# Performance work log

Hardware: AMD Instinct MI355X
Metric: run time of the kernel (lower is better)

The kernel has to match this reference:

```python
import jax, jax.numpy as jnp
import numpy as np

E = 1024
B, QL, KVL = 8, 2048, 2048


def setup_inputs() -> dict:
    key = jax.random.key(0)
    ks = jax.random.split(key, 12)
    s = 1.0 / np.sqrt(E)
    return {
        "query": jax.random.normal(ks[0], (B, QL, E), jnp.float32),
        "key_value": jax.random.normal(ks[1], (B, KVL, E), jnp.float32),
        "attention_mask": jax.random.randint(ks[2], (B, QL, KVL), 0, 2, jnp.int32),
        "Wq": jax.random.uniform(ks[3], (E, E), jnp.float32, -s, s),
        "bq": jax.random.uniform(ks[4], (E,), jnp.float32, -s, s),
        "Wk": jax.random.uniform(ks[5], (E, E), jnp.float32, -s, s),
        "bk": jax.random.uniform(ks[6], (E,), jnp.float32, -s, s),
        "Wv": jax.random.uniform(ks[7], (E, E), jnp.float32, -s, s),
        "bv": jax.random.uniform(ks[8], (E,), jnp.float32, -s, s),
        "Wo": jax.random.uniform(ks[9], (E, E), jnp.float32, -s, s),
        "bo": jax.random.uniform(ks[10], (E,), jnp.float32, -s, s),
    }


def reference(query, key_value, attention_mask, Wq, bq, Wk, bk, Wv, bv, Wo, bo):
    # torch Linear: x @ W.T + b
    q = jnp.einsum('bqe,fe->bqf', query, Wq) + bq          # [B, QL, E]
    k = jnp.einsum('bke,fe->bkf', key_value, Wk) + bk      # [B, KVL, E]
    v = jnp.einsum('bke,fe->bkf', key_value, Wv) + bv      # [B, KVL, E]
    scale = 1.0 / jnp.sqrt(jnp.asarray(q.shape[-1], q.dtype))
    attn = jnp.einsum('bqe,bke->bqk', q, k) * scale        # [B, QL, KVL]
    attn = jnp.where(attention_mask == 0, -jnp.inf, attn)
    attn = jax.nn.softmax(attn, axis=-1)
    out = jnp.einsum('bqk,bke->bqe', attn, v)              # [B, QL, E]
    out = jnp.einsum('bqe,fe->bqf', out, Wo) + bo
    return out
```

## Files before the change

kernel.cpp:

```cpp
#include <hip/hip_runtime.h>
#include <hip/hip_bf16.h>
#include <stdint.h>

typedef unsigned short u16;
typedef short s16x8 __attribute__((ext_vector_type(8)));
typedef u16 u16x8 __attribute__((ext_vector_type(8)));
typedef u16 u16x4 __attribute__((ext_vector_type(4)));
typedef float f32x4 __attribute__((ext_vector_type(4)));

__device__ __forceinline__ u16 f2bf(float f) {
  union { float f; uint32_t u; } c; c.f = f;
  uint32_t u = c.u;
  u = u + 0x7fffu + ((u >> 16) & 1u);
  return (u16)(u >> 16);
}
__device__ __forceinline__ float bf2f(u16 b) {
  union { uint32_t u; float f; } c; c.u = ((uint32_t)b) << 16;
  return c.f;
}

__device__ __forceinline__ void gld_lds16(const u16* g, u16* l) {
  __builtin_amdgcn_global_load_lds(
      (const __attribute__((address_space(1))) uint32_t*)g,
      (__attribute__((address_space(3))) uint32_t*)l,
      16, 0, 0);
}

__global__ __launch_bounds__(256) void cvt_wt(
    const float* __restrict__ Wq, const float* __restrict__ Wk,
    const float* __restrict__ Wv, const float* __restrict__ Wo,
    u16* __restrict__ WqT, u16* __restrict__ WkT, u16* __restrict__ WvT,
    u16* __restrict__ wo) {
  const int z = blockIdx.z;
  const int tid = threadIdx.x;
  if (z == 3) {
    const long base = ((long)(blockIdx.y * 16 + blockIdx.x)) * 4096 + tid * 16;
#pragma unroll
    for (int h = 0; h < 2; ++h) {
      const float4 a = *(const float4*)&Wo[base + h * 8];
      const float4 b = *(const float4*)&Wo[base + h * 8 + 4];
      u16x8 r;
      r[0] = f2bf(a.x); r[1] = f2bf(a.y); r[2] = f2bf(a.z); r[3] = f2bf(a.w);
      r[4] = f2bf(b.x); r[5] = f2bf(b.y); r[6] = f2bf(b.z); r[7] = f2bf(b.w);
      *(u16x8*)&wo[base + h * 8] = r;
    }
    return;
  }
  const float* src = (z == 0) ? Wq : (z == 1) ? Wk : Wv;
  u16* dst = (z == 0) ? WqT : (z == 1) ? WkT : WvT;
  __shared__ u16 t[64][66];
  const int r0 = blockIdx.x * 64, c0 = blockIdx.y * 64;
#pragma unroll
  for (int i = 0; i < 2; ++i) {
    const int ch = i * 256 + tid;
    const int r = ch >> 3, cc = ch & 7;
    const float4 a = *(const float4*)&src[(long)(r0 + r) * 1024 + c0 + cc * 8];
    const float4 b = *(const float4*)&src[(long)(r0 + r) * 1024 + c0 + cc * 8 + 4];
    t[r][cc * 8 + 0] = f2bf(a.x); t[r][cc * 8 + 1] = f2bf(a.y);
    t[r][cc * 8 + 2] = f2bf(a.z); t[r][cc * 8 + 3] = f2bf(a.w);
    t[r][cc * 8 + 4] = f2bf(b.x); t[r][cc * 8 + 5] = f2bf(b.y);
    t[r][cc * 8 + 6] = f2bf(b.z); t[r][cc * 8 + 7] = f2bf(b.w);
  }
  __syncthreads();
#pragma unroll
  for (int i = 0; i < 2; ++i) {
    const int ch = i * 256 + tid;
    const int c = ch >> 3, rr = ch & 7;
    u16x8 r8;
#pragma unroll
    for (int j = 0; j < 8; ++j) r8[j] = t[rr * 8 + j][c];
    *(u16x8*)&dst[(long)(c0 + c) * 1024 + r0 + rr * 8] = r8;
  }
}

__global__ __launch_bounds__(256) void bgemv(
    const u16* __restrict__ matA, const float* __restrict__ vecA,
    const u16* __restrict__ matB, const float* __restrict__ vecB,
    const float* __restrict__ addB, float* __restrict__ outA,
    float* __restrict__ outB, float scaleA) {
  __shared__ float w[1024];
  const int tid = threadIdx.x;
  const bool second = blockIdx.x >= 64;
  const u16* mat = second ? matB : matA;
  const float* vec = second ? vecB : vecA;
  const int rb = (second ? (int)blockIdx.x - 64 : (int)blockIdx.x) * 16;
#pragma unroll
  for (int i = 0; i < 4; ++i) w[i * 256 + tid] = vec[i * 256 + tid];
  __syncthreads();
  const int lane = tid & 63, wv_ = tid >> 6;
#pragma unroll
  for (int r = 0; r < 4; ++r) {
    const int row = rb + wv_ * 4 + r;
    const u16* p = &mat[(long)row * 1024 + lane * 16];
    const u16x8 a = *(const u16x8*)p;
    const u16x8 b = *(const u16x8*)(p + 8);
    float s = 0.f;
#pragma unroll
    for (int j = 0; j < 8; ++j) s += bf2f(a[j]) * w[lane * 16 + j];
#pragma unroll
    for (int j = 0; j < 8; ++j) s += bf2f(b[j]) * w[lane * 16 + 8 + j];
#pragma unroll
    for (int off = 32; off >= 1; off >>= 1) s += __shfl_xor(s, off);
    if (lane == 0) {
      if (second) outB[row] = s + addB[row];
      else        outA[row] = s * scaleA;
    }
  }
}

__global__ __launch_bounds__(256) void cvt_inputs(
    const float* __restrict__ kv, const float* __restrict__ query,
    const float* __restrict__ wvec, u16* __restrict__ kvbf,
    u16* __restrict__ qbf, float* __restrict__ cvec) {
  __shared__ float w[1024];
  const int tid = threadIdx.x;
  const bool qside = blockIdx.x >= 2048;
  if (!qside) {
#pragma unroll
    for (int i = 0; i < 4; ++i) w[i * 256 + tid] = wvec[i * 256 + tid];
    __syncthreads();
  }
  const int lane = tid & 63, wv_ = tid >> 6;
  const long blk = qside ? (long)blockIdx.x - 2048 : (long)blockIdx.x;
  const float* src_base = qside ? query : kv;
  u16* dst_base = qside ? qbf : kvbf;
#pragma unroll
  for (int r = 0; r < 2; ++r) {
    const long row = blk * 8 + wv_ * 2 + r;
    const float* src = &src_base[row * 1024 + lane * 16];
    const float4 a0 = *(const float4*)src;
    const float4 a1 = *(const float4*)(src + 4);
    const float4 a2 = *(const float4*)(src + 8);
    const float4 a3 = *(const float4*)(src + 12);
    u16x8 p0, p1;
    p0[0] = f2bf(a0.x); p0[1] = f2bf(a0.y); p0[2] = f2bf(a0.z); p0[3] = f2bf(a0.w);
    p0[4] = f2bf(a1.x); p0[5] = f2bf(a1.y); p0[6] = f2bf(a1.z); p0[7] = f2bf(a1.w);
    p1[0] = f2bf(a2.x); p1[1] = f2bf(a2.y); p1[2] = f2bf(a2.z); p1[3] = f2bf(a2.w);
    p1[4] = f2bf(a3.x); p1[5] = f2bf(a3.y); p1[6] = f2bf(a3.z); p1[7] = f2bf(a3.w);
    *(u16x8*)&dst_base[row * 1024 + lane * 16] = p0;
    *(u16x8*)&dst_base[row * 1024 + lane * 16 + 8] = p1;
    if (!qside) {
      const float* wl = &w[lane * 16];
      float s = a0.x * wl[0] + a0.y * wl[1] + a0.z * wl[2] + a0.w * wl[3]
              + a1.x * wl[4] + a1.y * wl[5] + a1.z * wl[6] + a1.w * wl[7]
              + a2.x * wl[8] + a2.y * wl[9] + a2.z * wl[10] + a2.w * wl[11]
              + a3.x * wl[12] + a3.y * wl[13] + a3.z * wl[14] + a3.w * wl[15];
#pragma unroll
      for (int off = 32; off >= 1; off >>= 1) s += __shfl_xor(s, off);
      if (lane == 0) cvec[row] = s;
    }
  }
}

__global__ __launch_bounds__(256) void softmax_rows(u16* __restrict__ S) {
  const long base = (long)blockIdx.x * 2048;
  const int tid = threadIdx.x;
  const int lane = tid & 63, wave = tid >> 6;
  u16x8 raw = *(const u16x8*)&S[base + tid * 8];
  float v[8];
#pragma unroll
  for (int j = 0; j < 8; ++j) v[j] = bf2f(raw[j]);
  float m = v[0];
#pragma unroll
  for (int j = 1; j < 8; ++j) m = fmaxf(m, v[j]);
#pragma unroll
  for (int off = 32; off >= 1; off >>= 1) m = fmaxf(m, __shfl_xor(m, off));
  __shared__ float red[8];
  if (lane == 0) red[wave] = m;
  __syncthreads();
  m = fmaxf(fmaxf(red[0], red[1]), fmaxf(red[2], red[3]));
  float s = 0.f;
#pragma unroll
  for (int j = 0; j < 8; ++j) { v[j] = __expf(v[j] - m); s += v[j]; }
#pragma unroll
  for (int off = 32; off >= 1; off >>= 1) s += __shfl_xor(s, off);
  if (lane == 0) red[4 + wave] = s;
  __syncthreads();
  s = (red[4] + red[5]) + (red[6] + red[7]);
  const float inv = 1.f / s;
#pragma unroll
  for (int j = 0; j < 8; ++j) raw[j] = f2bf(v[j] * inv);
  *(u16x8*)&S[base + tid * 8] = raw;
}

union __align__(16) SmemT {
  u16 stage[2][128 * 64];
  float epi[32 * 132];
};

__device__ __forceinline__ s16x8 ldsfrag(const u16* p, int r, int c8) {
  return *(const s16x8*)&p[r * 64 + ((c8 ^ (r & 7)) << 3)];
}

__device__ __forceinline__ void stage128(const u16* __restrict__ gb, int row0,
                                         int K, int k0, u16* lbuf, int tid) {
#pragma unroll
  for (int i = 0; i < 4; ++i) {
    const int f = i * 256 + tid;
    const int rl = f >> 3, s = f & 7;
    const int gc = (s ^ (rl & 7)) << 3;
    gld_lds16(gb + (long)(row0 + rl) * K + k0 + gc, lbuf + f * 8);
  }
}

template<bool HAS_BIAS, int MODE, bool HAS_MASK>
__global__ __launch_bounds__(256, 4) void gemm128(
    const u16* __restrict__ A, const u16* __restrict__ B,
    const float* __restrict__ bias, const int* __restrict__ mask,
    void* __restrict__ Cv,
    int M, int N, int K, long sA, long sB, long sC, long sMask, long sBias,
    float scale) {
  __shared__ SmemT sm;
  const int nx = gridDim.x, ny = gridDim.y;
  const int did = blockIdx.x + nx * (blockIdx.y + ny * blockIdx.z);
  const int cpx = (nx * ny * gridDim.z) >> 3;
  const int nf = (did & 7) * cpx + (did >> 3);
  const int b = nf / (nx * ny);
  const int rr = nf % (nx * ny);
  const int bm = (rr / ny) * 128;
  const int bn = (rr % ny) * 128;

  const u16* Ab = A + (long)b * sA;
  const u16* Bb = B + (long)b * sB;
  const float* biasB = HAS_BIAS ? (bias + (long)b * sBias) : nullptr;
  const int tid = threadIdx.x;
  const int lane = tid & 63, wave = tid >> 6;
  const int wm = wave >> 1, wn = wave & 1;
  const int lr = lane & 15, lk = lane >> 4;
  const int NT = K >> 6;

  f32x4 acc[4][4] = {};

  for (int t = 0; t < NT; ++t) {
    stage128(Ab, bm, K, t << 6, sm.stage[0], tid);
    stage128(Bb, bn, K, t << 6, sm.stage[1], tid);
    asm volatile("s_waitcnt vmcnt(0)" ::: "memory");
    __syncthreads();
#pragma unroll
    for (int ks = 0; ks < 2; ++ks) {
      s16x8 af[4], bg[4];
#pragma unroll
      for (int mi = 0; mi < 4; ++mi)
        af[mi] = ldsfrag(sm.stage[0], wm * 64 + mi * 16 + lr, ks * 4 + lk);
#pragma unroll
      for (int ni = 0; ni < 4; ++ni)
        bg[ni] = ldsfrag(sm.stage[1], wn * 64 + ni * 16 + lr, ks * 4 + lk);
#pragma unroll
      for (int mi = 0; mi < 4; ++mi)
#pragma unroll
        for (int ni = 0; ni < 4; ++ni)
          acc[mi][ni] = __builtin_amdgcn_mfma_f32_16x16x32_bf16(
              af[mi], bg[ni], acc[mi][ni], 0, 0, 0);
    }
    __syncthreads();
  }

  const long cb = (long)b * sC;
  const int q = tid & 7, r = tid >> 3;
#pragma unroll
  for (int h = 0; h < 4; ++h) {
    __syncthreads();
    if (wm == (h >> 1)) {
      const int mi0 = (h & 1) * 2;
#pragma unroll
      for (int mm = 0; mm < 2; ++mm) {
        const int mi = mi0 + mm;
#pragma unroll
        for (int ni = 0; ni < 4; ++ni) {
          const int c = wn * 64 + ni * 16 + lr;
          const float bvx = HAS_BIAS ? biasB[bn + c] : 0.f;
#pragma unroll
          for (int j = 0; j < 4; ++j)
            sm.epi[(mm * 16 + (lk << 2) + j) * 132 + c] =
                acc[mi][ni][j] * scale + bvx;
        }
      }
    }
    __syncthreads();
    const int growi = bm + h * 32 + r;
    const long grow = cb + (long)growi * N + bn;
    const long mrow = HAS_MASK
        ? ((long)b * sMask + (long)growi * (long)N + bn) : 0;
#pragma unroll
    for (int ch = 0; ch < 2; ++ch) {
      const int c0 = ch * 64 + q * 8;
      const float4 x = *(const float4*)&sm.epi[r * 132 + c0];
      const float4 y = *(const float4*)&sm.epi[r * 132 + c0 + 4];
      if (MODE == 1) {
        *(float4*)&((float*)Cv)[grow + c0] = x;
        *(float4*)&((float*)Cv)[grow + c0 + 4] = y;
      } else {
        u16x8 pk;
        if (HAS_MASK) {
          const int4 ma = *(const int4*)&mask[mrow + c0];
          const int4 mb = *(const int4*)&mask[mrow + c0 + 4];
          pk[0] = f2bf(ma.x ? x.x : -1e30f);
          pk[1] = f2bf(ma.y ? x.y : -1e30f);
          pk[2] = f2bf(ma.z ? x.z : -1e30f);
          pk[3] = f2bf(ma.w ? x.w : -1e30f);
          pk[4] = f2bf(mb.x ? y.x : -1e30f);
          pk[5] = f2bf(mb.y ? y.y : -1e30f);
          pk[6] = f2bf(mb.z ? y.z : -1e30f);
          pk[7] = f2bf(mb.w ? y.w : -1e30f);
        } else {
          pk[0] = f2bf(x.x); pk[1] = f2bf(x.y);
          pk[2] = f2bf(x.z); pk[3] = f2bf(x.w);
          pk[4] = f2bf(y.x); pk[5] = f2bf(y.y);
          pk[6] = f2bf(y.z); pk[7] = f2bf(y.w);
        }
        *(u16x8*)&((u16*)Cv)[grow + c0] = pk;
      }
    }
  }
}

extern "C" void kernel_launch(void* const* d_in, const int* in_sizes, int n_in,
                              void* d_out, int out_size, void* d_ws, size_t ws_size,
                              hipStream_t stream) {
  const float* query = (const float*)d_in[0];
  const float* kv    = (const float*)d_in[1];
  const int*   mask  = (const int*)d_in[2];
  const float* Wq = (const float*)d_in[3];
  const float* bq = (const float*)d_in[4];
  const float* Wk = (const float*)d_in[5];
  const float* bk = (const float*)d_in[6];
  const float* Wv = (const float*)d_in[7];
  const float* bv = (const float*)d_in[8];
  const float* Wo = (const float*)d_in[9];
  const float* bo = (const float*)d_in[10];
  float* out = (float*)d_out;
  (void)bk;

  char* ws = (char*)d_ws;
  const size_t MB = (size_t)1 << 20;
  u16* qbf  = (u16*)(ws + 0);
  u16* kvbf = (u16*)(ws + 32 * MB);
  u16* wo   = (u16*)(ws + 70 * MB);
  u16* WqT  = (u16*)(ws + 72 * MB);
  u16* WkT  = (u16*)(ws + 74 * MB);
  u16* WvT  = (u16*)(ws + 76 * MB);
  u16* Mt   = (u16*)(ws + 78 * MB);
  u16* Wvo  = (u16*)(ws + 80 * MB);
  float* wvec = (float*)(ws + 82 * MB);
  float* bvo  = (float*)(ws + 82 * MB + 65536);
  float* cvec = (float*)(ws + 83 * MB);
  u16* qM   = (u16*)(ws + 84 * MB);
  u16* VwT  = (u16*)(ws + 116 * MB);
  u16* S    = (u16*)(ws + 148 * MB);

  const long sQK = (long)2048 * 1024;
  const long sS  = (long)2048 * 2048;

  cvt_wt<<<dim3(16, 16, 4), 256, 0, stream>>>(Wq, Wk, Wv, Wo,
                                              WqT, WkT, WvT, wo);
  bgemv<<<128, 256, 0, stream>>>(WkT, bq, wo, bv, bo, wvec, bvo, 0.03125f);

  cvt_inputs<<<4096, 256, 0, stream>>>(kv, query, wvec, kvbf, qbf, cvec);

  gemm128<false, 0, false><<<dim3(8, 8, 2), 256, 0, stream>>>(
      WkT, WqT, nullptr, nullptr, Mt, 1024, 1024, 1024,
      -2097152L, 2097152L, 1048576L, 0, 0, 1.f);

  gemm128<false, 0, false><<<dim3(128, 8, 1), 256, 0, stream>>>(
      qbf, Mt, nullptr, nullptr, qM, 16384, 1024, 1024, 0, 0, 0, 0, 0, 1.f);

  gemm128<false, 0, false><<<dim3(8, 16, 8), 256, 0, stream>>>(
      Wvo, kvbf, nullptr, nullptr, VwT, 1024, 2048, 1024,
      0, sQK, sQK, 0, 0, 1.f);

  gemm128<true, 0, true><<<dim3(16, 16, 8), 256, 0, stream>>>(
      qM, kvbf, cvec, mask, S, 2048, 2048, 1024, sQK, sQK, sS, sS, 2048,
      0.03125f);

  softmax_rows<<<16384, 256, 0, stream>>>(S);

  gemm128<true, 1, false><<<dim3(16, 8, 8), 256, 0, stream>>>(
      S, VwT, bvo, nullptr, out, 2048, 1024, 2048, sS, sQK, sQK, 0, 0, 1.f);
}
```

Baseline: 333.1 us.

## Merge independent prep kernels into two heterogeneous fused launches

Replaces five separate launches (bgemv, cvt_inputs, the Mt GEMM, the qM GEMM and the VwT GEMM) with two kernels that dispatch by block index. One handles input conversion, the Mt GEMM and the bias GEMVs; the other handles the qM and VwT GEMMs plus the cvec GEMV, now computed from bf16 kv instead of fp32. The aim is to cut launch gaps and let independent work fill the GPU together. In exchange, every block now uses GEMM-sized shared memory, which may reduce occupancy for the light conversion blocks. cvec also loses precision because it is built from bf16 inputs.

```diff
diff --git a/kernel.cpp b/kernel.cpp
--- a/kernel.cpp
+++ b/kernel.cpp
@@ -5,7 +5,6 @@
 typedef unsigned short u16;
 typedef short s16x8 __attribute__((ext_vector_type(8)));
 typedef u16 u16x8 __attribute__((ext_vector_type(8)));
-typedef u16 u16x4 __attribute__((ext_vector_type(4)));
 typedef float f32x4 __attribute__((ext_vector_type(4)));
 
 __device__ __forceinline__ u16 f2bf(float f) {
@@ -73,85 +72,6 @@
   }
 }
 
-__global__ __launch_bounds__(256) void bgemv(
-    const u16* __restrict__ matA, const float* __restrict__ vecA,
-    const u16* __restrict__ matB, const float* __restrict__ vecB,
-    const float* __restrict__ addB, float* __restrict__ outA,
-    float* __restrict__ outB, float scaleA) {
-  __shared__ float w[1024];
-  const int tid = threadIdx.x;
-  const bool second = blockIdx.x >= 64;
-  const u16* mat = second ? matB : matA;
-  const float* vec = second ? vecB : vecA;
-  const int rb = (second ? (int)blockIdx.x - 64 : (int)blockIdx.x) * 16;
-#pragma unroll
-  for (int i = 0; i < 4; ++i) w[i * 256 + tid] = vec[i * 256 + tid];
-  __syncthreads();
-  const int lane = tid & 63, wv_ = tid >> 6;
-#pragma unroll
-  for (int r = 0; r < 4; ++r) {
-    const int row = rb + wv_ * 4 + r;
-    const u16* p = &mat[(long)row * 1024 + lane * 16];
-    const u16x8 a = *(const u16x8*)p;
-    const u16x8 b = *(const u16x8*)(p + 8);
-    float s = 0.f;
-#pragma unroll
-    for (int j = 0; j < 8; ++j) s += bf2f(a[j]) * w[lane * 16 + j];
-#pragma unroll
-    for (int j = 0; j < 8; ++j) s += bf2f(b[j]) * w[lane * 16 + 8 + j];
-#pragma unroll
-    for (int off = 32; off >= 1; off >>= 1) s += __shfl_xor(s, off);
-    if (lane == 0) {
-      if (second) outB[row] = s + addB[row];
-      else        outA[row] = s * scaleA;
-    }
-  }
-}
-
-__global__ __launch_bounds__(256) void cvt_inputs(
-    const float* __restrict__ kv, const float* __restrict__ query,
-    const float* __restrict__ wvec, u16* __restrict__ kvbf,
-    u16* __restrict__ qbf, float* __restrict__ cvec) {
-  __shared__ float w[1024];
-  const int tid = threadIdx.x;
-  const bool qside = blockIdx.x >= 2048;
-  if (!qside) {
-#pragma unroll
-    for (int i = 0; i < 4; ++i) w[i * 256 + tid] = wvec[i * 256 + tid];
-    __syncthreads();
-  }
-  const int lane = tid & 63, wv_ = tid >> 6;
-  const long blk = qside ? (long)blockIdx.x - 2048 : (long)blockIdx.x;
-  const float* src_base = qside ? query : kv;
-  u16* dst_base = qside ? qbf : kvbf;
-#pragma unroll
-  for (int r = 0; r < 2; ++r) {
-    const long row = blk * 8 + wv_ * 2 + r;
-    const float* src = &src_base[row * 1024 + lane * 16];
-    const float4 a0 = *(const float4*)src;
-    const float4 a1 = *(const float4*)(src + 4);
-    const float4 a2 = *(const float4*)(src + 8);
-    const float4 a3 = *(const float4*)(src + 12);
-    u16x8 p0, p1;
-    p0[0] = f2bf(a0.x); p0[1] = f2bf(a0.y); p0[2] = f2bf(a0.z); p0[3] = f2bf(a0.w);
-    p0[4] = f2bf(a1.x); p0[5] = f2bf(a1.y); p0[6] = f2bf(a1.z); p0[7] = f2bf(a1.w);
-    p1[0] = f2bf(a2.x); p1[1] = f2bf(a2.y); p1[2] = f2bf(a2.z); p1[3] = f2bf(a2.w);
-    p1[4] = f2bf(a3.x); p1[5] = f2bf(a3.y); p1[6] = f2bf(a3.z); p1[7] = f2bf(a3.w);
-    *(u16x8*)&dst_base[row * 1024 + lane * 16] = p0;
-    *(u16x8*)&dst_base[row * 1024 + lane * 16 + 8] = p1;
-    if (!qside) {
-      const float* wl = &w[lane * 16];
-      float s = a0.x * wl[0] + a0.y * wl[1] + a0.z * wl[2] + a0.w * wl[3]
-              + a1.x * wl[4] + a1.y * wl[5] + a1.z * wl[6] + a1.w * wl[7]
-              + a2.x * wl[8] + a2.y * wl[9] + a2.z * wl[10] + a2.w * wl[11]
-              + a3.x * wl[12] + a3.y * wl[13] + a3.z * wl[14] + a3.w * wl[15];
-#pragma unroll
-      for (int off = 32; off >= 1; off >>= 1) s += __shfl_xor(s, off);
-      if (lane == 0) cvec[row] = s;
-    }
-  }
-}
-
 __global__ __launch_bounds__(256) void softmax_rows(u16* __restrict__ S) {
   const long base = (long)blockIdx.x * 2048;
   const int tid = threadIdx.x;
@@ -204,16 +124,13 @@
 }
 
 template<bool HAS_BIAS, int MODE, bool HAS_MASK>
-__global__ __launch_bounds__(256, 4) void gemm128(
-    const u16* __restrict__ A, const u16* __restrict__ B,
+__device__ __forceinline__ void gemm128_body(
+    SmemT& sm, int tid, const u16* __restrict__ A, const u16* __restrict__ B,
     const float* __restrict__ bias, const int* __restrict__ mask,
-    void* __restrict__ Cv,
-    int M, int N, int K, long sA, long sB, long sC, long sMask, long sBias,
-    float scale) {
-  __shared__ SmemT sm;
-  const int nx = gridDim.x, ny = gridDim.y;
-  const int did = blockIdx.x + nx * (blockIdx.y + ny * blockIdx.z);
-  const int cpx = (nx * ny * gridDim.z) >> 3;
+    void* __restrict__ Cv, int M, int N, int K,
+    long sA, long sB, long sC, long sMask, long sBias, float scale,
+    int did, int nx, int ny, int nz) {
+  const int cpx = (nx * ny * nz) >> 3;
   const int nf = (did & 7) * cpx + (did >> 3);
   const int b = nf / (nx * ny);
   const int rr = nf % (nx * ny);
@@ -223,7 +140,6 @@
   const u16* Ab = A + (long)b * sA;
   const u16* Bb = B + (long)b * sB;
   const float* biasB = HAS_BIAS ? (bias + (long)b * sBias) : nullptr;
-  const int tid = threadIdx.x;
   const int lane = tid & 63, wave = tid >> 6;
   const int wm = wave >> 1, wn = wave & 1;
   const int lr = lane & 15, lk = lane >> 4;
@@ -314,6 +230,131 @@
   }
 }
 
+template<bool HAS_BIAS, int MODE, bool HAS_MASK>
+__global__ __launch_bounds__(256, 4) void gemm128(
+    const u16* __restrict__ A, const u16* __restrict__ B,
+    const float* __restrict__ bias, const int* __restrict__ mask,
+    void* __restrict__ Cv,
+    int M, int N, int K, long sA, long sB, long sC, long sMask, long sBias,
+    float scale) {
+  __shared__ SmemT sm;
+  const int did = blockIdx.x + gridDim.x * (blockIdx.y + gridDim.y * blockIdx.z);
+  gemm128_body<HAS_BIAS, MODE, HAS_MASK>(
+      sm, threadIdx.x, A, B, bias, mask, Cv, M, N, K, sA, sB, sC, sMask,
+      sBias, scale, did, gridDim.x, gridDim.y, gridDim.z);
+}
+
+__global__ __launch_bounds__(256, 4) void fused_prep(
+    const float* __restrict__ kv, const float* __restrict__ query,
+    u16* __restrict__ kvbf, u16* __restrict__ qbf,
+    const u16* __restrict__ WkT, const u16* __restrict__ WqT,
+    u16* __restrict__ Mt, const u16* __restrict__ wo,
+    const float* __restrict__ bq, const float* __restrict__ bv,
+    const float* __restrict__ bo, float* __restrict__ wvec,
+    float* __restrict__ bvo) {
+  __shared__ SmemT sm;
+  const int tid = threadIdx.x;
+  const int bid = blockIdx.x;
+  const int lane = tid & 63, wv_ = tid >> 6;
+  if (bid < 4096) {
+    const bool qside = bid >= 2048;
+    const long blk = qside ? bid - 2048 : bid;
+    const float* src_base = qside ? query : kv;
+    u16* dst_base = qside ? qbf : kvbf;
+#pragma unroll
+    for (int r = 0; r < 2; ++r) {
+      const long row = blk * 8 + wv_ * 2 + r;
+      const float* src = &src_base[row * 1024 + lane * 16];
+      const float4 a0 = *(const float4*)src;
+      const float4 a1 = *(const float4*)(src + 4);
+      const float4 a2 = *(const float4*)(src + 8);
+      const float4 a3 = *(const float4*)(src + 12);
+      u16x8 p0, p1;
+      p0[0] = f2bf(a0.x); p0[1] = f2bf(a0.y); p0[2] = f2bf(a0.z); p0[3] = f2bf(a0.w);
+      p0[4] = f2bf(a1.x); p0[5] = f2bf(a1.y); p0[6] = f2bf(a1.z); p0[7] = f2bf(a1.w);
+      p1[0] = f2bf(a2.x); p1[1] = f2bf(a2.y); p1[2] = f2bf(a2.z); p1[3] = f2bf(a2.w);
+      p1[4] = f2bf(a3.x); p1[5] = f2bf(a3.y); p1[6] = f2bf(a3.z); p1[7] = f2bf(a3.w);
+      *(u16x8*)&dst_base[row * 1024 + lane * 16] = p0;
+      *(u16x8*)&dst_base[row * 1024 + lane * 16 + 8] = p1;
+    }
+  } else if (bid < 4224) {
+    gemm128_body<false, 0, false>(
+        sm, tid, WkT, WqT, nullptr, nullptr, Mt, 1024, 1024, 1024,
+        -2097152L, 2097152L, 1048576L, 0, 0, 1.f, bid - 4096, 8, 8, 2);
+  } else {
+    const int sub = bid - 4224;
+    const bool second = sub >= 64;
+    const u16* mat = second ? wo : WkT;
+    const float* vec = second ? bv : bq;
+    const int rb = (second ? sub - 64 : sub) * 16;
+    float* w = sm.epi;
+#pragma unroll
+    for (int i = 0; i < 4; ++i) w[i * 256 + tid] = vec[i * 256 + tid];
+    __syncthreads();
+#pragma unroll
+    for (int r = 0; r < 4; ++r) {
+      const int row = rb + wv_ * 4 + r;
+      const u16* p = &mat[(long)row * 1024 + lane * 16];
+      const u16x8 a = *(const u16x8*)p;
+      const u16x8 b = *(const u16x8*)(p + 8);
+      float s = 0.f;
+#pragma unroll
+      for (int j = 0; j < 8; ++j) s += bf2f(a[j]) * w[lane * 16 + j];
+#pragma unroll
+      for (int j = 0; j < 8; ++j) s += bf2f(b[j]) * w[lane * 16 + 8 + j];
+#pragma unroll
+      for (int off = 32; off >= 1; off >>= 1) s += __shfl_xor(s, off);
+      if (lane == 0) {
+        if (second) bvo[row] = s + bo[row];
+        else        wvec[row] = s * 0.03125f;
+      }
+    }
+  }
+}
+
+__global__ __launch_bounds__(256, 4) void fused_mid(
+    const u16* __restrict__ qbf, const u16* __restrict__ Mt,
+    u16* __restrict__ qM, const u16* __restrict__ Wvo,
+    const u16* __restrict__ kvbf, u16* __restrict__ VwT,
+    const float* __restrict__ wvec, float* __restrict__ cvec) {
+  __shared__ SmemT sm;
+  const int tid = threadIdx.x;
+  const int bid = blockIdx.x;
+  if (bid < 2048) {
+    const bool isQM = bid < 1024;
+    gemm128_body<false, 0, false>(
+        sm, tid,
+        isQM ? qbf : Wvo, isQM ? Mt : kvbf, nullptr, nullptr,
+        isQM ? (void*)qM : (void*)VwT,
+        isQM ? 16384 : 1024, isQM ? 1024 : 2048, 1024,
+        0L, isQM ? 0L : 2097152L, isQM ? 0L : 2097152L, 0L, 0L, 1.f,
+        isQM ? bid : bid - 1024,
+        isQM ? 128 : 8, isQM ? 8 : 16, isQM ? 1 : 8);
+  } else {
+    const int lane = tid & 63, wv_ = tid >> 6;
+    float* w = sm.epi;
+#pragma unroll
+    for (int i = 0; i < 4; ++i) w[i * 256 + tid] = wvec[i * 256 + tid];
+    __syncthreads();
+    const long rowbase = (long)(bid - 2048) * 16 + wv_ * 4;
+#pragma unroll
+    for (int r = 0; r < 4; ++r) {
+      const long row = rowbase + r;
+      const u16* p = &kvbf[row * 1024 + lane * 16];
+      const u16x8 a = *(const u16x8*)p;
+      const u16x8 b = *(const u16x8*)(p + 8);
+      float s = 0.f;
+#pragma unroll
+      for (int j = 0; j < 8; ++j) s += bf2f(a[j]) * w[lane * 16 + j];
+#pragma unroll
+      for (int j = 0; j < 8; ++j) s += bf2f(b[j]) * w[lane * 16 + 8 + j];
+#pragma unroll
+      for (int off = 32; off >= 1; off >>= 1) s += __shfl_xor(s, off);
+      if (lane == 0) cvec[row] = s;
+    }
+  }
+}
+
 extern "C" void kernel_launch(void* const* d_in, const int* in_sizes, int n_in,
                               void* d_out, int out_size, void* d_ws, size_t ws_size,
                               hipStream_t stream) {
@@ -353,20 +394,13 @@
 
   cvt_wt<<<dim3(16, 16, 4), 256, 0, stream>>>(Wq, Wk, Wv, Wo,
                                               WqT, WkT, WvT, wo);
-  bgemv<<<128, 256, 0, stream>>>(WkT, bq, wo, bv, bo, wvec, bvo, 0.03125f);
-
-  cvt_inputs<<<4096, 256, 0, stream>>>(kv, query, wvec, kvbf, qbf, cvec);
-
-  gemm128<false, 0, false><<<dim3(8, 8, 2), 256, 0, stream>>>(
-      WkT, WqT, nullptr, nullptr, Mt, 1024, 1024, 1024,
-      -2097152L, 2097152L, 1048576L, 0, 0, 1.f);
-
-  gemm128<false, 0, false><<<dim3(128, 8, 1), 256, 0, stream>>>(
-      qbf, Mt, nullptr, nullptr, qM, 16384, 1024, 1024, 0, 0, 0, 0, 0, 1.f);
-
-  gemm128<false, 0, false><<<dim3(8, 16, 8), 256, 0, stream>>>(
-      Wvo, kvbf, nullptr, nullptr, VwT, 1024, 2048, 1024,
-      0, sQK, sQK, 0, 0, 1.f);
+
+  fused_prep<<<4352, 256, 0, stream>>>(kv, query, kvbf, qbf,
+                                       WkT, WqT, Mt, wo, bq, bv, bo,
+                                       wvec, bvo);
+
+  fused_mid<<<3072, 256, 0, stream>>>(qbf, Mt, qM, Wvo, kvbf, VwT,
+                                      wvec, cvec);
 
   gemm128<true, 0, true><<<dim3(16, 16, 8), 256, 0, stream>>>(
       qM, kvbf, cvec, mask, S, 2048, 2048, 1024, sQK, sQK, sS, sS, 2048,
```

Result: faster. 316.8 us (median of 2 runs) (-4.9%).
